# Kernel tuning notes

Measured on AMD Instinct MI355X. Metric: run time of the kernel, lower is better.

## Reference

```python
import jax, jax.numpy as jnp
import numpy as np

D_MODEL = 1024
NUM_HEADS = 16
D_K = D_MODEL // NUM_HEADS
ROPE_THETA = 10000.0


def _rope(x, positions):
    # x: [B, H, S, Dk]; positions: [S] int. Interleaved-pair RoPE, theta=10000.
    half = D_K // 2
    inv_freq = 1.0 / (ROPE_THETA ** (jnp.arange(half, dtype=jnp.float32) * 2.0 / D_K))
    ang = positions.astype(jnp.float32)[:, None] * inv_freq[None, :]  # [S, half]
    cos = jnp.cos(ang)[None, None]  # [1,1,S,half]
    sin = jnp.sin(ang)[None, None]
    x_even = x[..., 0::2]
    x_odd = x[..., 1::2]
    r_even = x_even * cos - x_odd * sin
    r_odd = x_even * sin + x_odd * cos
    out = jnp.stack([r_even, r_odd], axis=-1)  # [B,H,S,half,2]
    return out.reshape(x.shape)


def setup_inputs() -> dict:
    key = jax.random.key(0)
    ks = jax.random.split(key, 5)
    B, S = 4, 2048
    std = (2.0 / (D_MODEL + D_MODEL)) ** 0.5
    return {
        "x": jax.random.normal(ks[0], (B, S, D_MODEL), dtype=jnp.float32),
        "Wq": jax.random.normal(ks[1], (D_MODEL, D_MODEL), dtype=jnp.float32) * std,
        "Wk": jax.random.normal(ks[2], (D_MODEL, D_MODEL), dtype=jnp.float32) * std,
        "Wv": jax.random.normal(ks[3], (D_MODEL, D_MODEL), dtype=jnp.float32) * std,
        "Wo": jax.random.normal(ks[4], (D_MODEL, D_MODEL), dtype=jnp.float32) * std,
        "token_positions": jnp.arange(S, dtype=jnp.int32),
    }


def reference(x, Wq, Wk, Wv, Wo, token_positions):
    B, S, _ = x.shape
    # QKV projections (weights stored [out, in], y = x @ W^T)
    def proj(W):
        y = jnp.einsum('bsi,oi->bso', x, W)
        return y.reshape(B, S, NUM_HEADS, D_K).transpose(0, 2, 1, 3)  # [B,H,S,Dk]
    q = _rope(proj(Wq), token_positions)
    k = _rope(proj(Wk), token_positions)
    v = proj(Wv)
    scores = jnp.einsum('bhqd,bhkd->bhqk', q, k) / jnp.sqrt(jnp.float32(D_K))
    causal = token_positions[:, None] >= token_positions[None, :]  # [S,S]
    scores = jnp.where(causal[None, None], scores, jnp.float32(-1e9))
    probs = jax.nn.softmax(scores, axis=-1)
    attn = jnp.einsum('bhqk,bhkd->bhqd', probs, v)
    attn = attn.transpose(0, 2, 1, 3).reshape(B, S, D_MODEL)
    return jnp.einsum('bsi,oi->bso', attn, Wo)
```

## Files before the change

### kernel.cpp

```cpp
#include <hip/hip_runtime.h>
#include <hip/hip_bf16.h>
#include <math.h>

#define SEQ 2048
#define BATCH 4
#define MROWS (BATCH*SEQ)
#define DMODEL 1024
#define NHEADS 16
#define DKH 64

typedef float f32x4 __attribute__((ext_vector_type(4)));
typedef float f32x16 __attribute__((ext_vector_type(16)));
typedef __bf16 bf16x8 __attribute__((ext_vector_type(8)));
typedef unsigned short u16;
typedef unsigned int u32;
typedef u16 u16x4 __attribute__((ext_vector_type(4)));
typedef u16 u16x8 __attribute__((ext_vector_type(8)));
typedef u32 u32x4v __attribute__((ext_vector_type(4)));

__device__ __forceinline__ u16 f2bf(float f) {
  union { float f; unsigned u; } v; v.f = f;
  unsigned r = v.u + 0x7FFFu + ((v.u >> 16) & 1u);
  return (u16)(r >> 16);
}

__device__ __forceinline__ void async_copy16(const void* g, void* l) {
  __builtin_amdgcn_global_load_lds(
      (const __attribute__((address_space(1))) void*)g,
      (__attribute__((address_space(3))) void*)l, 16, 0, 0);
}

__device__ __forceinline__ u32 cvtpk(float lo, float hi) {
  u32 r;
  asm("v_cvt_pk_bf16_f32 %0, %1, %2" : "=v"(r) : "v"(lo), "v"(hi));
  return r;
}

__global__ __launch_bounds__(256) void k_prep(
    const float* __restrict__ x,
    const float* __restrict__ Wq, const float* __restrict__ Wk,
    const float* __restrict__ Wv, const float* __restrict__ Wo,
    const int* __restrict__ pos,
    u16* __restrict__ xb, u16* __restrict__ Wqb, u16* __restrict__ Wkb,
    u16* __restrict__ Wvb, u16* __restrict__ Wob,
    float* __restrict__ cosT, float* __restrict__ sinT)
{
  const int bid = blockIdx.x, tid = threadIdx.x;
  if (bid < 8192) {
    int i = bid*256 + tid;
    float4 v = ((const float4*)x)[i];
    u16x4 o; o[0]=f2bf(v.x); o[1]=f2bf(v.y); o[2]=f2bf(v.z); o[3]=f2bf(v.w);
    ((u16x4*)xb)[i] = o;
  } else if (bid < 12288) {
    int wi = (bid - 8192) >> 10;
    const float* src = (wi==0)?Wq:(wi==1)?Wk:(wi==2)?Wv:Wo;
    u16* dst = (wi==0)?Wqb:(wi==1)?Wkb:(wi==2)?Wvb:Wob;
    int i = ((bid - 8192) & 1023)*256 + tid;
    float4 v = ((const float4*)src)[i];
    u16x4 o; o[0]=f2bf(v.x); o[1]=f2bf(v.y); o[2]=f2bf(v.z); o[3]=f2bf(v.w);
    ((u16x4*)dst)[i] = o;
  } else {
    int i = (bid - 12288)*256 + tid;
    int s = i >> 5, j = i & 31;
    double p = (double)pos[s];
    double inv = pow(10000.0, -(double)j / 32.0);
    double a = p * inv;
    cosT[i] = (float)cos(a);
    sinT[i] = (float)sin(a);
  }
}

template<int MODE>
__global__ __launch_bounds__(256) void k_gemm_all(
    const u16* __restrict__ A,
    const u16* __restrict__ W0, const u16* __restrict__ W1,
    const u16* __restrict__ W2,
    u16* __restrict__ Qo, u16* __restrict__ Ko, u16* __restrict__ Vto,
    float* __restrict__ Fo,
    const float* __restrict__ cosT, const float* __restrict__ sinT)
{
  __shared__ u16 Asl[128*32];
  __shared__ u16 Bsl[128*32];
  const int bm = blockIdx.x, bn = blockIdx.y;
  const int tid = threadIdx.x;
  const int wave = tid >> 6, lane = tid & 63;
  const int lg = lane >> 4, lr = lane & 15;
  const int wm = wave >> 1, wn = wave & 1;

  int proj, bnl;
  const u16* W;
  if constexpr (MODE == 0) {
    proj = bn >> 3; bnl = bn & 7;
    W = (proj == 0) ? W0 : (proj == 1) ? W1 : W2;
  } else {
    proj = 3; bnl = bn; W = W0;
  }

  f32x4 acc[4][4];
#pragma unroll
  for (int i = 0; i < 4; ++i)
#pragma unroll
    for (int j = 0; j < 4; ++j) acc[i][j] = (f32x4){0,0,0,0};

  const int srow = lane >> 2;
  const int sk8  = (lane & 3) * 8;

  for (int kt = 0; kt < 32; ++kt) {
    const int k0 = kt * 32;
#pragma unroll
    for (int i = 0; i < 2; ++i) {
      const u16* ga = A + (size_t)(bm*128 + i*64 + wave*16 + srow)*DMODEL + k0 + sk8;
      const u16* gb = W + (size_t)(bnl*128 + i*64 + wave*16 + srow)*DMODEL + k0 + sk8;
      async_copy16(ga, (char*)Asl + i*4096 + wave*1024);
      async_copy16(gb, (char*)Bsl + i*4096 + wave*1024);
    }
    __syncthreads();
    bf16x8 af[4], bfr[4];
#pragma unroll
    for (int mi = 0; mi < 4; ++mi)
      af[mi] = *(const bf16x8*)&Asl[(wm*64 + mi*16 + lr)*32 + lg*8];
#pragma unroll
    for (int ni = 0; ni < 4; ++ni)
      bfr[ni] = *(const bf16x8*)&Bsl[(wn*64 + ni*16 + lr)*32 + lg*8];
#pragma unroll
    for (int mi = 0; mi < 4; ++mi)
#pragma unroll
      for (int ni = 0; ni < 4; ++ni)
        acc[mi][ni] = __builtin_amdgcn_mfma_f32_16x16x32_bf16(af[mi], bfr[ni], acc[mi][ni], 0, 0, 0);
    __syncthreads();
  }

#pragma unroll
  for (int mi = 0; mi < 4; ++mi) {
    const int row0 = bm*128 + wm*64 + mi*16 + lg*4;
#pragma unroll
    for (int ni = 0; ni < 4; ++ni) {
      const int col = bnl*128 + wn*64 + ni*16 + lr;
      f32x4 a = acc[mi][ni];
      if constexpr (MODE == 1) {
#pragma unroll
        for (int r = 0; r < 4; ++r) Fo[(size_t)(row0+r)*DMODEL + col] = a[r];
      } else {
        if (proj == 2) {
          const int hh = col >> 6, dd = col & 63;
          const int s0r = row0 & (SEQ-1);
          const int bb = row0 >> 11;
          u16x4 wv;
#pragma unroll
          for (int r = 0; r < 4; ++r) wv[r] = f2bf(a[r]);
          *(u16x4*)&Vto[((size_t)((bb*16+hh)*64 + dd))*SEQ + s0r] = wv;
        } else {
          u16* C = (proj == 0) ? Qo : Ko;
          const float scl = (proj == 0) ? 0.18033688f : 1.0f;
          const int dd = col & 63;
          const int j = dd >> 1;
          const float sgn = (dd & 1) ? 1.0f : -1.0f;
#pragma unroll
          for (int r = 0; r < 4; ++r) {
            const int s = (row0 + r) & (SEQ-1);
            float v = a[r];
            float pv = __shfl_xor(v, 1, 64);
            float c = cosT[s*32 + j], sn = sinT[s*32 + j];
            C[(size_t)(row0+r)*DMODEL + col] = f2bf((v*c + sgn*pv*sn) * scl);
          }
        }
      }
    }
  }
}

__global__ __launch_bounds__(512) void k_attn(
    const u16* __restrict__ Q, const u16* __restrict__ K,
    const u16* __restrict__ Vt, u16* __restrict__ O)
{
  const int bh = blockIdx.x;
  const int qt = (gridDim.y - 1) - blockIdx.y;
  const int b = bh >> 4, h = bh & 15;
  const int wave = threadIdx.x >> 6, lane = threadIdx.x & 63;
  const int ql = lane & 31, hi = lane >> 5, hi4 = hi * 4;
  const int R0 = qt*256 + wave*32;

  __shared__ alignas(16) u16 Ks[2][64*64];
  __shared__ alignas(16) u16 Vs[2][64*64];

  const u16* Qb = Q + (size_t)(b*SEQ)*DMODEL + h*64;
  const u16* Kb = K + (size_t)(b*SEQ)*DMODEL + h*64;
  const u16* Vb = Vt + (size_t)(bh*64)*SEQ;

  bf16x8 qf[4];
#pragma unroll
  for (int j = 0; j < 4; ++j)
    qf[j] = *(const bf16x8*)(Qb + (size_t)(R0 + ql)*DMODEL + j*16 + hi*8);

  union { u16x8 u; bf16x8 v; } onesu;
#pragma unroll
  for (int i = 0; i < 8; ++i) onesu.u[i] = 0x3F80;
  const bf16x8 ones = onesu.v;

  f32x16 o0 = (f32x16)(0.f), o1 = (f32x16)(0.f);
  f32x16 lacc = (f32x16)(0.f);
  float m_run = -INFINITY;
  const float THR2 = 11.5415603f;

  const int KT = (qt + 1) * 4;

  const int qp = (ql & ~12) | ((ql & 4) << 1) | ((ql & 8) >> 1);

  auto stage = [&](int buf, int kt) {
    const int idx = threadIdx.x;
    const int row = idx >> 3, ch = idx & 7;
    const int sch = (ch ^ (row & 7)) * 8;
    const int k0 = kt * 64;
    async_copy16(Kb + (size_t)(k0 + row)*DMODEL + sch, (char*)Ks[buf] + idx*16);
    async_copy16(Vb + (size_t)row*SEQ + k0 + sch,      (char*)Vs[buf] + idx*16);
  };

  stage(0, 0);
  __syncthreads();

  for (int kt = 0; kt < KT; ++kt) {
    const int cur = kt & 1;
    if (kt + 1 < KT) stage(cur ^ 1, kt + 1);

    const int k0 = kt*64;
    if (k0 <= R0 + 31) {
      const u16* Kw = Ks[cur];
      const u16* Vw = Vs[cur];

      bf16x8 ka[2][4];
#pragma unroll
      for (int st = 0; st < 2; ++st)
#pragma unroll
        for (int j = 0; j < 4; ++j) {
          const int rk = st*32 + qp;
          const int c = (2*j + hi) ^ (rk & 7);
          ka[st][j] = *(const bf16x8*)&Kw[rk*64 + c*8];
        }
      f32x16 s0 = (f32x16)(0.f), s1 = (f32x16)(0.f);
#pragma unroll
      for (int j = 0; j < 4; ++j) {
        s0 = __builtin_amdgcn_mfma_f32_32x32x16_bf16(ka[0][j], qf[j], s0, 0, 0, 0);
        s1 = __builtin_amdgcn_mfma_f32_32x32x16_bf16(ka[1][j], qf[j], s1, 0, 0, 0);
      }

      if (k0 + 63 > R0) {
        const int base = k0 - R0;
#pragma unroll
        for (int r = 0; r < 16; ++r) {
          const int kl = (r & 7) + (hi << 3) + ((r & 8) << 1);
          s0[r] = (ql >= base + kl)      ? s0[r] : -1e30f;
          s1[r] = (ql >= base + 32 + kl) ? s1[r] : -1e30f;
        }
      }

      float t[16];
#pragma unroll
      for (int r = 0; r < 16; ++r) t[r] = fmaxf(s0[r], s1[r]);
#pragma unroll
      for (int w = 8; w >= 1; w >>= 1)
#pragma unroll
        for (int r = 0; r < w; ++r) t[r] = fmaxf(t[r], t[r+w]);
      const float mx = fmaxf(t[0], __shfl_xor(t[0], 32, 64));

      if (__any(mx > m_run + THR2)) {
        const float mn = fmaxf(m_run, mx);
        const float al = __builtin_exp2f(m_run - mn);
        m_run = mn;
        lacc[0] *= al;
#pragma unroll
        for (int r = 0; r < 16; ++r) { o0[r] *= al; o1[r] *= al; }
      }

      float e0[16], e1[16];
#pragma unroll
      for (int r = 0; r < 16; ++r) {
        e0[r] = __builtin_exp2f(s0[r] - m_run);
        e1[r] = __builtin_exp2f(s1[r] - m_run);
      }

      bf16x8 pb[4];
#pragma unroll
      for (int sl = 0; sl < 4; ++sl) {
        const float* e = (sl < 2) ? e0 : e1;
        const int o8 = (sl & 1) * 8;
        u32 w0 = cvtpk(e[o8+0], e[o8+1]);
        u32 w1 = cvtpk(e[o8+2], e[o8+3]);
        u32 w2 = cvtpk(e[o8+4], e[o8+5]);
        u32 w3 = cvtpk(e[o8+6], e[o8+7]);
        union { u32x4v u; bf16x8 v; } uu;
        uu.u = (u32x4v){w0, w1, w2, w3};
        pb[sl] = uu.v;
      }

#pragma unroll
      for (int sl = 0; sl < 4; ++sl) {
        const int c0 = 2*sl + hi;
        const int d0 = ql,      ca = (c0 ^ (d0 & 7));
        const int d1 = 32 + ql, cb = (c0 ^ (d1 & 7));
        bf16x8 va0 = *(const bf16x8*)&Vw[d0*64 + ca*8];
        bf16x8 va1 = *(const bf16x8*)&Vw[d1*64 + cb*8];
        o0 = __builtin_amdgcn_mfma_f32_32x32x16_bf16(va0, pb[sl], o0, 0, 0, 0);
        o1 = __builtin_amdgcn_mfma_f32_32x32x16_bf16(va1, pb[sl], o1, 0, 0, 0);
        lacc = __builtin_amdgcn_mfma_f32_32x32x16_bf16(ones, pb[sl], lacc, 0, 0, 0);
      }
    }
    __syncthreads();
  }

  const float inv = 1.0f / lacc[0];
  u16* Orow = O + (size_t)(b*SEQ + R0 + ql)*DMODEL + h*64;
#pragma unroll
  for (int rb = 0; rb < 4; ++rb) {
    u16x4 wA, wB;
#pragma unroll
    for (int j = 0; j < 4; ++j) {
      wA[j] = f2bf(o0[rb*4 + j] * inv);
      wB[j] = f2bf(o1[rb*4 + j] * inv);
    }
    *(u16x4*)(Orow + 8*rb + hi4)      = wA;
    *(u16x4*)(Orow + 32 + 8*rb + hi4) = wB;
  }
}

extern "C" void kernel_launch(void* const* d_in, const int* in_sizes, int n_in,
                              void* d_out, int out_size, void* d_ws, size_t ws_size,
                              hipStream_t stream) {
  const float* x  = (const float*)d_in[0];
  const float* Wq = (const float*)d_in[1];
  const float* Wk = (const float*)d_in[2];
  const float* Wv = (const float*)d_in[3];
  const float* Wo = (const float*)d_in[4];
  const int* pos  = (const int*)d_in[5];
  float* out = (float*)d_out;

  const size_t SZ_X   = (size_t)MROWS*DMODEL*2;
  const size_t SZ_W   = (size_t)DMODEL*DMODEL*2;
  const size_t SZ_TAB = (size_t)SEQ*32*4;
  char* w = (char*)d_ws;
  u16* xb   = (u16*)(w);
  u16* Wqb  = (u16*)(w + SZ_X);
  u16* Wkb  = (u16*)(w + SZ_X + SZ_W);
  u16* Wvb  = (u16*)(w + SZ_X + 2*SZ_W);
  u16* Wob  = (u16*)(w + SZ_X + 3*SZ_W);
  float* cosT = (float*)(w + SZ_X + 4*SZ_W);
  float* sinT = (float*)(w + SZ_X + 4*SZ_W + SZ_TAB);
  u16* Qb   = (u16*)(w + SZ_X + 4*SZ_W + 2*SZ_TAB);
  u16* Kb   = (u16*)(w + 2*SZ_X + 4*SZ_W + 2*SZ_TAB);
  u16* Ob   = (u16*)(w + 3*SZ_X + 4*SZ_W + 2*SZ_TAB);
  u16* Vt   = (u16*)(w + 4*SZ_X + 4*SZ_W + 2*SZ_TAB);
  const size_t need = 5*SZ_X + 4*SZ_W + 2*SZ_TAB;
  if (ws_size < need) return;

  k_prep<<<12544, 256, 0, stream>>>(x, Wq, Wk, Wv, Wo, pos,
                                    xb, Wqb, Wkb, Wvb, Wob, cosT, sinT);
  k_gemm_all<0><<<dim3(MROWS/128, 24), 256, 0, stream>>>(
      xb, Wqb, Wkb, Wvb, Qb, Kb, Vt, nullptr, cosT, sinT);
  k_attn<<<dim3(BATCH*NHEADS, SEQ/256), 512, 0, stream>>>(Qb, Kb, Vt, Ob);
  k_gemm_all<1><<<dim3(MROWS/128, 8), 256, 0, stream>>>(
      Ob, Wob, nullptr, nullptr, nullptr, nullptr, nullptr, out, cosT, sinT);
}
```

Measured before the change: 205.0 us.

## Rewrite projection GEMMs with 128x256 tiles, triple-buffered async loads and swizzled LDS

The QKV and output projection GEMMs move to 512-thread blocks computing 128x256 tiles with BK=64. Global-to-LDS copies are triple-buffered and issued two stages ahead, with explicit vmcnt waits, so loads overlap MFMA work. An XOR swizzle on the LDS layout removes bank conflicts, and setprio raises the priority of the MFMA sections. In exchange, LDS use grows to about 144KB per block, which limits occupancy, and the grid has fewer blocks.

```diff
diff --git a/kernel.cpp b/kernel.cpp
--- a/kernel.cpp
+++ b/kernel.cpp
@@ -71,7 +71,7 @@
 }
 
 template<int MODE>
-__global__ __launch_bounds__(256) void k_gemm_all(
+__global__ __launch_bounds__(512) void k_gemm2(
     const u16* __restrict__ A,
     const u16* __restrict__ W0, const u16* __restrict__ W1,
     const u16* __restrict__ W2,
@@ -79,22 +79,26 @@
     float* __restrict__ Fo,
     const float* __restrict__ cosT, const float* __restrict__ sinT)
 {
-  __shared__ u16 Asl[128*32];
-  __shared__ u16 Bsl[128*32];
-  const int bm = blockIdx.x, bn = blockIdx.y;
+  __shared__ alignas(16) u16 As[3][128*64];
+  __shared__ alignas(16) u16 Bs[3][256*64];
+
+  const int bm = blockIdx.x;
+  int proj, bnl;
+  const u16* W;
+  if constexpr (MODE == 0) {
+    proj = blockIdx.y >> 2; bnl = blockIdx.y & 3;
+    W = (proj == 0) ? W0 : (proj == 1) ? W1 : W2;
+  } else {
+    proj = 3; bnl = blockIdx.y; W = W0;
+  }
+
   const int tid = threadIdx.x;
   const int wave = tid >> 6, lane = tid & 63;
   const int lg = lane >> 4, lr = lane & 15;
-  const int wm = wave >> 1, wn = wave & 1;
-
-  int proj, bnl;
-  const u16* W;
-  if constexpr (MODE == 0) {
-    proj = bn >> 3; bnl = bn & 7;
-    W = (proj == 0) ? W0 : (proj == 1) ? W1 : W2;
-  } else {
-    proj = 3; bnl = bn; W = W0;
-  }
+  const int wm = wave >> 2, wn = wave & 3;
+
+  const u16* Ab = A + (size_t)(bm*128)*DMODEL;
+  const u16* Wb = W + (size_t)(bnl*256)*DMODEL;
 
   f32x4 acc[4][4];
 #pragma unroll
@@ -102,32 +106,66 @@
 #pragma unroll
     for (int j = 0; j < 4; ++j) acc[i][j] = (f32x4){0,0,0,0};
 
-  const int srow = lane >> 2;
-  const int sk8  = (lane & 3) * 8;
-
-  for (int kt = 0; kt < 32; ++kt) {
-    const int k0 = kt * 32;
+  auto stage = [&](int buf, int kt) {
+    const int k0 = kt * 64;
 #pragma unroll
     for (int i = 0; i < 2; ++i) {
-      const u16* ga = A + (size_t)(bm*128 + i*64 + wave*16 + srow)*DMODEL + k0 + sk8;
-      const u16* gb = W + (size_t)(bnl*128 + i*64 + wave*16 + srow)*DMODEL + k0 + sk8;
-      async_copy16(ga, (char*)Asl + i*4096 + wave*1024);
-      async_copy16(gb, (char*)Bsl + i*4096 + wave*1024);
-    }
-    __syncthreads();
-    bf16x8 af[4], bfr[4];
-#pragma unroll
-    for (int mi = 0; mi < 4; ++mi)
-      af[mi] = *(const bf16x8*)&Asl[(wm*64 + mi*16 + lr)*32 + lg*8];
-#pragma unroll
-    for (int ni = 0; ni < 4; ++ni)
-      bfr[ni] = *(const bf16x8*)&Bsl[(wn*64 + ni*16 + lr)*32 + lg*8];
-#pragma unroll
-    for (int mi = 0; mi < 4; ++mi)
-#pragma unroll
-      for (int ni = 0; ni < 4; ++ni)
-        acc[mi][ni] = __builtin_amdgcn_mfma_f32_16x16x32_bf16(af[mi], bfr[ni], acc[mi][ni], 0, 0, 0);
-    __syncthreads();
+      const int idx = i*512 + tid;
+      const int row = idx >> 3, ch = idx & 7;
+      async_copy16(Ab + (size_t)row*DMODEL + k0 + ((ch ^ (row & 7)) * 8),
+                   (char*)As[buf] + idx*16);
+    }
+#pragma unroll
+    for (int i = 0; i < 4; ++i) {
+      const int idx = i*512 + tid;
+      const int row = idx >> 3, ch = idx & 7;
+      async_copy16(Wb + (size_t)row*DMODEL + k0 + ((ch ^ (row & 7)) * 8),
+                   (char*)Bs[buf] + idx*16);
+    }
+  };
+
+  const int NT = DMODEL / 64;
+  stage(0, 0);
+  stage(1, 1);
+  asm volatile("s_waitcnt vmcnt(6)" ::: "memory");
+  __builtin_amdgcn_sched_barrier(0);
+  __builtin_amdgcn_s_barrier();
+
+  for (int t = 0; t < NT; ++t) {
+    const int cur = t % 3;
+    if (t + 2 < NT) stage((t + 2) % 3, t + 2);
+
+    const u16* Aw = As[cur];
+    const u16* Bw = Bs[cur];
+    __builtin_amdgcn_s_setprio(1);
+#pragma unroll
+    for (int kk = 0; kk < 2; ++kk) {
+      bf16x8 bfr[4];
+#pragma unroll
+      for (int ni = 0; ni < 4; ++ni) {
+        const int row = wn*64 + ni*16 + lr;
+        bfr[ni] = *(const bf16x8*)&Bw[row*64 + (((kk*4 + lg) ^ (row & 7)) * 8)];
+      }
+#pragma unroll
+      for (int mi = 0; mi < 4; ++mi) {
+        const int row = wm*64 + mi*16 + lr;
+        bf16x8 af = *(const bf16x8*)&Aw[row*64 + (((kk*4 + lg) ^ (row & 7)) * 8)];
+#pragma unroll
+        for (int ni = 0; ni < 4; ++ni)
+          acc[mi][ni] = __builtin_amdgcn_mfma_f32_16x16x32_bf16(af, bfr[ni], acc[mi][ni], 0, 0, 0);
+      }
+    }
+    __builtin_amdgcn_s_setprio(0);
+
+    if (t + 1 < NT) {
+      if (t + 2 < NT) {
+        asm volatile("s_waitcnt vmcnt(6)" ::: "memory");
+      } else {
+        asm volatile("s_waitcnt vmcnt(0)" ::: "memory");
+      }
+      __builtin_amdgcn_sched_barrier(0);
+      __builtin_amdgcn_s_barrier();
+    }
   }
 
 #pragma unroll
@@ -135,7 +173,7 @@
     const int row0 = bm*128 + wm*64 + mi*16 + lg*4;
 #pragma unroll
     for (int ni = 0; ni < 4; ++ni) {
-      const int col = bnl*128 + wn*64 + ni*16 + lr;
+      const int col = bnl*256 + wn*64 + ni*16 + lr;
       f32x4 a = acc[mi][ni];
       if constexpr (MODE == 1) {
 #pragma unroll
@@ -353,9 +391,9 @@
 
   k_prep<<<12544, 256, 0, stream>>>(x, Wq, Wk, Wv, Wo, pos,
                                     xb, Wqb, Wkb, Wvb, Wob, cosT, sinT);
-  k_gemm_all<0><<<dim3(MROWS/128, 24), 256, 0, stream>>>(
+  k_gemm2<0><<<dim3(MROWS/128, 12), 512, 0, stream>>>(
       xb, Wqb, Wkb, Wvb, Qb, Kb, Vt, nullptr, cosT, sinT);
   k_attn<<<dim3(BATCH*NHEADS, SEQ/256), 512, 0, stream>>>(Qb, Kb, Vt, Ob);
-  k_gemm_all<1><<<dim3(MROWS/128, 8), 256, 0, stream>>>(
+  k_gemm2<1><<<dim3(MROWS/128, 4), 512, 0, stream>>>(
       Ob, Wob, nullptr, nullptr, nullptr, nullptr, nullptr, out, cosT, sinT);
 }
```

Result: faster. 200.1 us (-2.4%).
